# Performance work log

Measured on AMD Instinct MI355X. Metric: run time of the kernel, lower is better.

## Reference

```python
import jax, jax.numpy as jnp
import numpy as np

B, N, H = 8, 2048, 1024

def setup_inputs() -> dict:
    key = jax.random.key(0)
    ks = jax.random.split(key, 10)
    s = 1.0 / np.sqrt(2 * H)
    return {
        "sem": jax.random.normal(ks[0], (B, N, H), jnp.float32),
        "temp": jax.random.normal(ks[1], (B, N, H), jnp.float32),
        "Wq": jax.random.normal(ks[2], (2 * H, H), jnp.float32) * s,
        "bq": jnp.zeros((H,), jnp.float32),
        "Wk": jax.random.normal(ks[3], (2 * H, H), jnp.float32) * s,
        "bk": jnp.zeros((H,), jnp.float32),
        "Wv": jax.random.normal(ks[4], (2 * H, H), jnp.float32) * s,
        "bv": jnp.zeros((H,), jnp.float32),
        "Wg": jax.random.normal(ks[5], (2 * H, 1), jnp.float32) * s,
        "bg": jnp.zeros((1,), jnp.float32),
    }

def reference(sem, temp, Wq, bq, Wk, bk, Wv, bv, Wg, bg):
    combined = jnp.concatenate([sem, temp], axis=-1)          # [B,N,2H]
    Q = combined @ Wq + bq                                    # [B,N,H]
    K = combined @ Wk + bk
    V = combined @ Wv + bv
    scale = 1.0 / jnp.sqrt(jnp.asarray(Q.shape[-1], Q.dtype))
    scores = jnp.einsum('bqh,bkh->bqk', Q, K) * scale         # [B,N,N]
    attn = jax.nn.softmax(scores, axis=-1)
    gate = jax.nn.sigmoid(combined @ Wg + bg)                 # [B,N,1]
    attn_weights = attn * gate                                # row-wise gate
    fused = jnp.einsum('bqk,bkh->bqh', attn_weights, V)       # [B,N,H]
    return fused + sem, attn_weights.mean(axis=1)             # [B,N,H], [B,N]
```

## Files before the change

### kernel.cpp

```cpp
#include <hip/hip_runtime.h>
#include <stdint.h>
#include <math.h>

#define NB 8
#define NN 2048
#define HH 1024
#define K2 2048
#define MM 16384

typedef unsigned short u16;
typedef __attribute__((ext_vector_type(8))) short short8v;
typedef __attribute__((ext_vector_type(4))) float floatx4;

__device__ __forceinline__ float bf2f(u16 u) { return __uint_as_float(((unsigned)u) << 16); }
__device__ __forceinline__ u16 f2bf(float f) {
  unsigned u = __float_as_uint(f);
  unsigned r = (u + 0x7fffu + ((u >> 16) & 1u)) >> 16;
  return (u16)r;
}

__device__ __forceinline__ void async16(const void* g, void* lds) {
  __builtin_amdgcn_global_load_lds((const __attribute__((address_space(1))) void*)g,
                                   (__attribute__((address_space(3))) void*)lds,
                                   16, 0, 0);
}

__device__ __forceinline__ int xcd_swz(int bid, int nblk) {
  return (bid & 7) * (nblk >> 3) + (bid >> 3);
}

#define SBAR() __builtin_amdgcn_sched_barrier(0)

__device__ __forceinline__ void gemm128_core(const u16* __restrict__ A, int lda,
                                             const u16* __restrict__ Bt, int ldb,
                                             int rowA0, int rowB0, int K,
                                             u16* sA, u16* sB, floatx4 acc[4][4]) {
  const int t = threadIdx.x;
  const int w = t >> 6, l = t & 63;
  const int wr = w >> 1, wc = w & 1;

#pragma unroll
  for (int mi = 0; mi < 4; mi++)
#pragma unroll
    for (int ni = 0; ni < 4; ni++) { floatx4 z = {0.f,0.f,0.f,0.f}; acc[mi][ni] = z; }

  const int srow = l >> 2;
  const int cs = (((l & 3) ^ ((l >> 3) & 3)) << 3);
  const u16* gA0 = A + (size_t)(rowA0 + w * 32 + srow) * lda + cs;
  const u16* gA1 = A + (size_t)(rowA0 + w * 32 + 16 + srow) * lda + cs;
  const u16* gB0 = Bt + (size_t)(rowB0 + w * 32 + srow) * ldb + cs;
  const u16* gB1 = Bt + (size_t)(rowB0 + w * 32 + 16 + srow) * ldb + cs;
  char* dA = (char*)sA + w * 2048 + l * 16;
  char* dB = (char*)sB + w * 2048 + l * 16;

  const int fr = l & 15;
  const int ch = (((l >> 4) ^ ((fr >> 1) & 3)) << 4);
  const int abase = wr * 4096 + fr * 64 + ch;
  const int bbase = wc * 4096 + fr * 64 + ch;

  const int NT = K >> 5;

#define STG128(bi, kt) { const int ko_ = (kt) << 5; const int bo_ = (bi) << 13; \
    async16(gA0 + ko_, dA + bo_); async16(gA1 + ko_, dA + bo_ + 1024);          \
    async16(gB0 + ko_, dB + bo_); async16(gB1 + ko_, dB + bo_ + 1024); }

  STG128(0, 0);
  for (int tt = 0; tt < NT; ++tt) {
    const int bc = tt & 1;
    if (tt + 1 < NT) {
      STG128(bc ^ 1, tt + 1);
      asm volatile("s_waitcnt vmcnt(4)" ::: "memory");
    } else {
      asm volatile("s_waitcnt vmcnt(0)" ::: "memory");
    }
    __builtin_amdgcn_s_barrier();

    const char* a = (const char*)sA + (bc << 13);
    const char* b = (const char*)sB + (bc << 13);
    short8v af[4], bf[4];
#pragma unroll
    for (int mi = 0; mi < 4; mi++) af[mi] = *(const short8v*)(a + abase + mi * 1024);
#pragma unroll
    for (int ni = 0; ni < 4; ni++) bf[ni] = *(const short8v*)(b + bbase + ni * 1024);
    __builtin_amdgcn_s_setprio(1);
#pragma unroll
    for (int mi = 0; mi < 4; mi++)
#pragma unroll
      for (int ni = 0; ni < 4; ni++)
        acc[mi][ni] = __builtin_amdgcn_mfma_f32_16x16x32_bf16(af[mi], bf[ni], acc[mi][ni], 0, 0, 0);
    __builtin_amdgcn_s_setprio(0);
    SBAR();
    __builtin_amdgcn_s_barrier();
  }
#undef STG128
}

__global__ void __launch_bounds__(256) k_prep_gate(const float* __restrict__ sem,
                                                   const float* __restrict__ temp,
                                                   const float* __restrict__ Wg,
                                                   const float* __restrict__ bg,
                                                   u16* __restrict__ X, float* __restrict__ gate) {
  __shared__ float red[4];
  int t = threadIdx.x, w = t >> 6, l = t & 63;
  float4 wa = *(const float4*)(Wg + t * 4);
  float4 wb = *(const float4*)(Wg + 1024 + t * 4);
  float bgv = bg[0];
  int row0 = blockIdx.x * 8;
  for (int rr = 0; rr < 8; rr++) {
    int row = row0 + rr;
    const float* s0 = sem + (size_t)row * 1024 + t * 4;
    const float* t0 = temp + (size_t)row * 1024 + t * 4;
    u16* xr = X + (size_t)row * 2048;
    float4 a = *(const float4*)s0;
    float4 b = *(const float4*)t0;
    ushort4 oa = { f2bf(a.x), f2bf(a.y), f2bf(a.z), f2bf(a.w) };
    ushort4 ob = { f2bf(b.x), f2bf(b.y), f2bf(b.z), f2bf(b.w) };
    *(ushort4*)(xr + t * 4) = oa;
    *(ushort4*)(xr + 1024 + t * 4) = ob;
    float s = a.x * wa.x + a.y * wa.y + a.z * wa.z + a.w * wa.w
            + b.x * wb.x + b.y * wb.y + b.z * wb.z + b.w * wb.w;
#pragma unroll
    for (int off = 32; off > 0; off >>= 1) s += __shfl_xor(s, off);
    if (l == 0) red[w] = s;
    __syncthreads();
    if (t == 0) {
      float tot = red[0] + red[1] + red[2] + red[3] + bgv;
      gate[row] = 1.f / (1.f + expf(-tot));
    }
    __syncthreads();
  }
}

__global__ void __launch_bounds__(256) k_transpose_w3(const float* __restrict__ Wq,
                                                      const float* __restrict__ Wk,
                                                      const float* __restrict__ Wv,
                                                      u16* __restrict__ Wt) {
  __shared__ float s[32][33];
  int tile = blockIdx.x;
  int which = tile >> 11; tile &= 2047;
  const float* W = which == 0 ? Wq : which == 1 ? Wk : Wv;
  u16* dst = Wt + (size_t)which * 1024 * 2048;
  int nt = tile & 31, kt = tile >> 5;
  int tx = threadIdx.x & 31, ty = threadIdx.x >> 5;
  int n0 = nt << 5, k0 = kt << 5;
#pragma unroll
  for (int j = 0; j < 32; j += 8)
    s[ty + j][tx] = W[(size_t)(k0 + ty + j) * 1024 + (n0 + tx)];
  __syncthreads();
#pragma unroll
  for (int j = 0; j < 32; j += 8)
    dst[(size_t)(n0 + ty + j) * 2048 + (k0 + tx)] = f2bf(s[tx][ty + j]);
}

__global__ void __launch_bounds__(256, 4) k_proj_qkv(const u16* __restrict__ X,
                                                     const u16* __restrict__ Wt,
                                                     const float* __restrict__ bq,
                                                     const float* __restrict__ bk,
                                                     const float* __restrict__ bv,
                                                     u16* __restrict__ Qb,
                                                     u16* __restrict__ Kb,
                                                     u16* __restrict__ Vt) {
  __shared__ __align__(16) u16 sA[2 * 4096];
  __shared__ __align__(16) u16 sB[2 * 4096];
  int tile = xcd_swz(blockIdx.x, 3072);
  int bm = tile / 24, bn = tile - bm * 24;
  floatx4 acc[4][4];
  gemm128_core(X, K2, Wt, K2, bm * 128, bn * 128, K2, sA, sB, acc);

  const int t = threadIdx.x, w = t >> 6, l = t & 63;
  const int wr = w >> 1, wc = w & 1;
  const int r0 = bm * 128 + wr * 64 + ((l >> 4) << 2);
  const int c0 = (bn & 7) * 128 + wc * 64 + (l & 15);
  const int which = bn >> 3;
  if (which == 2) {
#pragma unroll
    for (int ni = 0; ni < 4; ni++) {
      int h = c0 + ni * 16;
      float bvv = bv[h];
#pragma unroll
      for (int mi = 0; mi < 4; mi++) {
        int rg = r0 + mi * 16;
        int b = rg >> 11, n = rg & 2047;
        ushort4 o = { f2bf(acc[mi][ni][0] + bvv), f2bf(acc[mi][ni][1] + bvv),
                      f2bf(acc[mi][ni][2] + bvv), f2bf(acc[mi][ni][3] + bvv) };
        *(ushort4*)&Vt[((size_t)b * 1024 + h) * 2048 + n] = o;
      }
    }
  } else {
    u16* Out = (which == 0) ? Qb : Kb;
    const float* bias = (which == 0) ? bq : bk;
#pragma unroll
    for (int ni = 0; ni < 4; ni++) {
      int c1 = c0 + ni * 16;
      float bvv = bias[c1];
#pragma unroll
      for (int mi = 0; mi < 4; mi++)
#pragma unroll
        for (int i = 0; i < 4; i++)
          Out[(size_t)(r0 + mi * 16 + i) * 1024 + c1] = f2bf(acc[mi][ni][i] + bvv);
    }
  }
}

__global__ void __launch_bounds__(256, 4) k_scores(const u16* __restrict__ Q, const u16* __restrict__ Kb,
                                                   u16* __restrict__ E, float* __restrict__ lsum) {
  __shared__ __align__(16) u16 sA[2 * 4096];
  __shared__ __align__(16) u16 sB[2 * 4096];
  int tile = xcd_swz(blockIdx.x, 2048);
  int b = tile >> 8, r = tile & 255, bm = r >> 4, bn = r & 15;
  const u16* A = Q + (size_t)b * NN * HH;
  const u16* Bt = Kb + (size_t)b * NN * HH;
  floatx4 acc[4][4];
  gemm128_core(A, HH, Bt, HH, bm * 128, bn * 128, HH, sA, sB, acc);

  u16* Eb = E + (size_t)b * NN * NN;
  float* lb = lsum + b * NN;
  const int t = threadIdx.x, w = t >> 6, l = t & 63;
  const int wr = w >> 1, wc = w & 1;
  const int q0 = bm * 128 + wr * 64 + ((l >> 4) << 2);
  const int k0c = bn * 128 + wc * 64 + (l & 15);
#pragma unroll
  for (int mi = 0; mi < 4; mi++)
#pragma unroll
    for (int i = 0; i < 4; i++) {
      int q = q0 + mi * 16 + i;
      float rs = 0.f;
#pragma unroll
      for (int ni = 0; ni < 4; ni++) {
        float e = expf(acc[mi][ni][i] * 0.03125f);
        Eb[(size_t)q * NN + k0c + ni * 16] = f2bf(e);
        rs += e;
      }
      rs += __shfl_xor(rs, 1);
      rs += __shfl_xor(rs, 2);
      rs += __shfl_xor(rs, 4);
      rs += __shfl_xor(rs, 8);
      if ((l & 15) == 0) atomicAdd(&lb[q], rs);
    }
}

__global__ void __launch_bounds__(256, 4) k_pv(const u16* __restrict__ E, const u16* __restrict__ Vt,
                                               const float* __restrict__ gate, const float* __restrict__ lsum,
                                               const float* __restrict__ sem, float* __restrict__ out) {
  __shared__ __align__(16) u16 sA[2 * 4096];
  __shared__ __align__(16) u16 sB[2 * 4096];
  int tile = xcd_swz(blockIdx.x, 1024);
  int b = tile >> 7, r = tile & 127, bm = r >> 3, bn = r & 7;
  const u16* A = E + (size_t)b * NN * NN;
  const u16* Bt = Vt + (size_t)b * HH * NN;
  floatx4 acc[4][4];
  gemm128_core(A, NN, Bt, NN, bm * 128, bn * 128, NN, sA, sB, acc);

  const int t = threadIdx.x, w = t >> 6, l = t & 63;
  const int wr = w >> 1, wc = w & 1;
  const int q0 = bm * 128 + wr * 64 + ((l >> 4) << 2);
  const int h0 = bn * 128 + wc * 64 + (l & 15);
#pragma unroll
  for (int mi = 0; mi < 4; mi++)
#pragma unroll
    for (int i = 0; i < 4; i++) {
      int q = q0 + mi * 16 + i;
      size_t gq = (size_t)b * NN + q;
      float wq = gate[gq] / lsum[gq];
#pragma unroll
      for (int ni = 0; ni < 4; ni++) {
        int h = h0 + ni * 16;
        out[gq * HH + h] = acc[mi][ni][i] * wq + sem[gq * HH + h];
      }
    }
}

__global__ void __launch_bounds__(256) k_colmean(const u16* __restrict__ E, const float* __restrict__ gate,
                                                 const float* __restrict__ lsum, float* __restrict__ cm) {
  __shared__ float wsh[256];
  int bid = blockIdx.x;
  int b = bid >> 5, rest = bid & 31;
  int ks = rest >> 3, qc = rest & 7;
  int t = threadIdx.x;
  {
    size_t gq = (size_t)b * NN + qc * 256 + t;
    wsh[t] = gate[gq] / lsum[gq];
  }
  __syncthreads();
  const u16* Eb = E + ((size_t)b * NN + (size_t)qc * 256) * NN + ks * 512 + 2 * t;
  float s0 = 0.f, s1 = 0.f;
#pragma unroll 4
  for (int q = 0; q < 256; q++) {
    unsigned v = *(const unsigned*)(Eb + (size_t)q * NN);
    float wq = wsh[q];
    s0 += wq * __uint_as_float(v << 16);
    s1 += wq * __uint_as_float(v & 0xffff0000u);
  }
  float* c = cm + b * NN + ks * 512 + 2 * t;
  atomicAdd(c, s0 * (1.f / 2048.f));
  atomicAdd(c + 1, s1 * (1.f / 2048.f));
}

extern "C" void kernel_launch(void* const* d_in, const int* in_sizes, int n_in,
                              void* d_out, int out_size, void* d_ws, size_t ws_size,
                              hipStream_t stream) {
  const float* sem  = (const float*)d_in[0];
  const float* temp = (const float*)d_in[1];
  const float* Wq   = (const float*)d_in[2];
  const float* bq   = (const float*)d_in[3];
  const float* Wk   = (const float*)d_in[4];
  const float* bk   = (const float*)d_in[5];
  const float* Wv   = (const float*)d_in[6];
  const float* bv   = (const float*)d_in[7];
  const float* Wg   = (const float*)d_in[8];
  const float* bg   = (const float*)d_in[9];
  float* out = (float*)d_out;

  char* ws = (char*)d_ws;
  u16* X      = (u16*)ws;
  u16* E      = X;
  u16* WqkvT  = (u16*)(ws + 67108864);
  u16* Qb     = (u16*)(ws + 79691776);
  u16* Kb     = (u16*)(ws + 113246208);
  u16* Vt     = (u16*)(ws + 146800640);
  float* gate = (float*)(ws + 180355072);
  float* lsum = (float*)(ws + 180420608);

  hipMemsetAsync(lsum, 0, 65536, stream);
  hipMemsetAsync(out + 16777216, 0, 65536, stream);

  k_prep_gate<<<2048, 256, 0, stream>>>(sem, temp, Wg, bg, X, gate);
  k_transpose_w3<<<6144, 256, 0, stream>>>(Wq, Wk, Wv, WqkvT);
  k_proj_qkv<<<3072, 256, 0, stream>>>(X, WqkvT, bq, bk, bv, Qb, Kb, Vt);
  k_scores<<<2048, 256, 0, stream>>>(Qb, Kb, E, lsum);
  k_pv<<<1024, 256, 0, stream>>>(E, Vt, gate, lsum, sem, out);
  k_colmean<<<256, 256, 0, stream>>>(E, gate, lsum, out + 16777216);
}
```

Measured before the change: 502.6 us.

## Store Q, K, V and exp-scores as FP8 and run attention GEMMs with FP8 MFMA

```diff
diff --git a/kernel.cpp b/kernel.cpp
--- a/kernel.cpp
+++ b/kernel.cpp
@@ -9,6 +9,7 @@
 #define MM 16384
 
 typedef unsigned short u16;
+typedef unsigned char u8;
 typedef __attribute__((ext_vector_type(8))) short short8v;
 typedef __attribute__((ext_vector_type(4))) float floatx4;
 
@@ -17,6 +18,33 @@
   unsigned u = __float_as_uint(f);
   unsigned r = (u + 0x7fffu + ((u >> 16) & 1u)) >> 16;
   return (u16)r;
+}
+
+__device__ __forceinline__ u8 f2fp8(float f) {
+  unsigned u = __float_as_uint(f);
+  unsigned sgn = (u >> 24) & 0x80u;
+  unsigned mag = u & 0x7fffffffu;
+  if (mag >= 0x43E80000u) return (u8)(sgn | 0x7Eu);
+  int e = (int)(mag >> 23) - 127;
+  unsigned m = mag & 0x7fffffu;
+  if (e < -6) {
+    float af = __uint_as_float(mag);
+    int q = (int)(af * 512.f + 0.5f);
+    if (q >= 8) return (u8)(sgn | 0x08u);
+    return (u8)(sgn | (unsigned)q);
+  }
+  unsigned r = m + 0x7FFFFu + ((m >> 20) & 1u);
+  unsigned m3 = r >> 20;
+  if (m3 >= 8u) { m3 = 0u; e++; }
+  if (e > 8 || (e == 8 && m3 == 7u)) return (u8)(sgn | 0x7Eu);
+  return (u8)(sgn | ((unsigned)(e + 7) << 3) | m3);
+}
+
+__device__ __forceinline__ float fp8dec(int x) {
+  int e = (x >> 3) & 15, m = x & 7;
+  float v = e ? __uint_as_float(((unsigned)(e - 7 + 127) << 23) | ((unsigned)m << 20))
+              : (float)m * 0.001953125f;
+  return (x & 0x80) ? -v : v;
 }
 
 __device__ __forceinline__ void async16(const void* g, void* lds) {
@@ -93,6 +121,84 @@
     __builtin_amdgcn_s_barrier();
   }
 #undef STG128
+}
+
+__device__ __forceinline__ void gemm128_fp8(const u8* __restrict__ A, int lda,
+                                            const u8* __restrict__ Bt, int ldb,
+                                            int rowA0, int rowB0, int K,
+                                            u8* sA, u8* sB, floatx4 acc[4][4]) {
+  const int t = threadIdx.x;
+  const int w = t >> 6, l = t & 63;
+  const int wr = w >> 1, wc = w & 1;
+
+#pragma unroll
+  for (int mi = 0; mi < 4; mi++)
+#pragma unroll
+    for (int ni = 0; ni < 4; ni++) { floatx4 z = {0.f,0.f,0.f,0.f}; acc[mi][ni] = z; }
+
+  const int srow = l >> 2;
+  const int cs = (((l & 3) ^ ((l >> 3) & 3)) << 4);
+  const u8* gA0 = A + (size_t)(rowA0 + w * 32 + srow) * lda + cs;
+  const u8* gA1 = A + (size_t)(rowA0 + w * 32 + 16 + srow) * lda + cs;
+  const u8* gB0 = Bt + (size_t)(rowB0 + w * 32 + srow) * ldb + cs;
+  const u8* gB1 = Bt + (size_t)(rowB0 + w * 32 + 16 + srow) * ldb + cs;
+  char* dA = (char*)sA + w * 2048 + l * 16;
+  char* dB = (char*)sB + w * 2048 + l * 16;
+
+  const int fr = l & 15;
+  const int g = l >> 4;
+  const int x = (fr >> 1) & 3;
+  const int c0 = ((((g >> 1) ^ x) << 4) | ((g & 1) << 3));
+  const int c1 = ((((2 + (g >> 1)) ^ x) << 4) | ((g & 1) << 3));
+  const int arow = wr * 4096 + fr * 64;
+  const int brow = wc * 4096 + fr * 64;
+
+  const int NT = K >> 6;
+
+#define STGF(bi, kt) { const int ko_ = (kt) << 6; const int bo_ = (bi) << 13; \
+    async16(gA0 + ko_, dA + bo_); async16(gA1 + ko_, dA + bo_ + 1024);        \
+    async16(gB0 + ko_, dB + bo_); async16(gB1 + ko_, dB + bo_ + 1024); }
+
+  STGF(0, 0);
+  for (int tt = 0; tt < NT; ++tt) {
+    const int bc = tt & 1;
+    if (tt + 1 < NT) {
+      STGF(bc ^ 1, tt + 1);
+      asm volatile("s_waitcnt vmcnt(4)" ::: "memory");
+    } else {
+      asm volatile("s_waitcnt vmcnt(0)" ::: "memory");
+    }
+    __builtin_amdgcn_s_barrier();
+
+    const char* a = (const char*)sA + (bc << 13);
+    const char* b = (const char*)sB + (bc << 13);
+    long a0[4], a1[4], b0[4], b1[4];
+#pragma unroll
+    for (int mi = 0; mi < 4; mi++) {
+      a0[mi] = *(const long*)(a + arow + mi * 1024 + c0);
+      a1[mi] = *(const long*)(a + arow + mi * 1024 + c1);
+    }
+#pragma unroll
+    for (int ni = 0; ni < 4; ni++) {
+      b0[ni] = *(const long*)(b + brow + ni * 1024 + c0);
+      b1[ni] = *(const long*)(b + brow + ni * 1024 + c1);
+    }
+    __builtin_amdgcn_s_setprio(1);
+#pragma unroll
+    for (int mi = 0; mi < 4; mi++)
+#pragma unroll
+      for (int ni = 0; ni < 4; ni++)
+        acc[mi][ni] = __builtin_amdgcn_mfma_f32_16x16x32_fp8_fp8(a0[mi], b0[ni], acc[mi][ni], 0, 0, 0);
+#pragma unroll
+    for (int mi = 0; mi < 4; mi++)
+#pragma unroll
+      for (int ni = 0; ni < 4; ni++)
+        acc[mi][ni] = __builtin_amdgcn_mfma_f32_16x16x32_fp8_fp8(a1[mi], b1[ni], acc[mi][ni], 0, 0, 0);
+    __builtin_amdgcn_s_setprio(0);
+    SBAR();
+    __builtin_amdgcn_s_barrier();
+  }
+#undef STGF
 }
 
 __global__ void __launch_bounds__(256) k_prep_gate(const float* __restrict__ sem,
@@ -157,9 +263,9 @@
                                                      const float* __restrict__ bq,
                                                      const float* __restrict__ bk,
                                                      const float* __restrict__ bv,
-                                                     u16* __restrict__ Qb,
-                                                     u16* __restrict__ Kb,
-                                                     u16* __restrict__ Vt) {
+                                                     u8* __restrict__ Qb,
+                                                     u8* __restrict__ Kb,
+                                                     u8* __restrict__ Vt) {
   __shared__ __align__(16) u16 sA[2 * 4096];
   __shared__ __align__(16) u16 sB[2 * 4096];
   int tile = xcd_swz(blockIdx.x, 3072);
@@ -181,13 +287,13 @@
       for (int mi = 0; mi < 4; mi++) {
         int rg = r0 + mi * 16;
         int b = rg >> 11, n = rg & 2047;
-        ushort4 o = { f2bf(acc[mi][ni][0] + bvv), f2bf(acc[mi][ni][1] + bvv),
-                      f2bf(acc[mi][ni][2] + bvv), f2bf(acc[mi][ni][3] + bvv) };
-        *(ushort4*)&Vt[((size_t)b * 1024 + h) * 2048 + n] = o;
+        uchar4 o = { f2fp8(acc[mi][ni][0] + bvv), f2fp8(acc[mi][ni][1] + bvv),
+                     f2fp8(acc[mi][ni][2] + bvv), f2fp8(acc[mi][ni][3] + bvv) };
+        *(uchar4*)&Vt[((size_t)b * 1024 + h) * 2048 + n] = o;
       }
     }
   } else {
-    u16* Out = (which == 0) ? Qb : Kb;
+    u8* Out = (which == 0) ? Qb : Kb;
     const float* bias = (which == 0) ? bq : bk;
 #pragma unroll
     for (int ni = 0; ni < 4; ni++) {
@@ -197,23 +303,23 @@
       for (int mi = 0; mi < 4; mi++)
 #pragma unroll
         for (int i = 0; i < 4; i++)
-          Out[(size_t)(r0 + mi * 16 + i) * 1024 + c1] = f2bf(acc[mi][ni][i] + bvv);
-    }
-  }
-}
-
-__global__ void __launch_bounds__(256, 4) k_scores(const u16* __restrict__ Q, const u16* __restrict__ Kb,
-                                                   u16* __restrict__ E, float* __restrict__ lsum) {
-  __shared__ __align__(16) u16 sA[2 * 4096];
-  __shared__ __align__(16) u16 sB[2 * 4096];
+          Out[(size_t)(r0 + mi * 16 + i) * 1024 + c1] = f2fp8(acc[mi][ni][i] + bvv);
+    }
+  }
+}
+
+__global__ void __launch_bounds__(256, 4) k_scores(const u8* __restrict__ Q, const u8* __restrict__ Kb,
+                                                   u8* __restrict__ E, float* __restrict__ lsum) {
+  __shared__ __align__(16) u8 sA[2 * 8192];
+  __shared__ __align__(16) u8 sB[2 * 8192];
   int tile = xcd_swz(blockIdx.x, 2048);
   int b = tile >> 8, r = tile & 255, bm = r >> 4, bn = r & 15;
-  const u16* A = Q + (size_t)b * NN * HH;
-  const u16* Bt = Kb + (size_t)b * NN * HH;
+  const u8* A = Q + (size_t)b * NN * HH;
+  const u8* Bt = Kb + (size_t)b * NN * HH;
   floatx4 acc[4][4];
-  gemm128_core(A, HH, Bt, HH, bm * 128, bn * 128, HH, sA, sB, acc);
-
-  u16* Eb = E + (size_t)b * NN * NN;
+  gemm128_fp8(A, HH, Bt, HH, bm * 128, bn * 128, HH, sA, sB, acc);
+
+  u8* Eb = E + (size_t)b * NN * NN;
   float* lb = lsum + b * NN;
   const int t = threadIdx.x, w = t >> 6, l = t & 63;
   const int wr = w >> 1, wc = w & 1;
@@ -228,8 +334,9 @@
 #pragma unroll
       for (int ni = 0; ni < 4; ni++) {
         float e = expf(acc[mi][ni][i] * 0.03125f);
-        Eb[(size_t)q * NN + k0c + ni * 16] = f2bf(e);
-        rs += e;
+        u8 c = f2fp8(e * 0.25f);
+        Eb[(size_t)q * NN + k0c + ni * 16] = c;
+        rs += fp8dec(c);
       }
       rs += __shfl_xor(rs, 1);
       rs += __shfl_xor(rs, 2);
@@ -239,17 +346,17 @@
     }
 }
 
-__global__ void __launch_bounds__(256, 4) k_pv(const u16* __restrict__ E, const u16* __restrict__ Vt,
+__global__ void __launch_bounds__(256, 4) k_pv(const u8* __restrict__ E, const u8* __restrict__ Vt,
                                                const float* __restrict__ gate, const float* __restrict__ lsum,
                                                const float* __restrict__ sem, float* __restrict__ out) {
-  __shared__ __align__(16) u16 sA[2 * 4096];
-  __shared__ __align__(16) u16 sB[2 * 4096];
+  __shared__ __align__(16) u8 sA[2 * 8192];
+  __shared__ __align__(16) u8 sB[2 * 8192];
   int tile = xcd_swz(blockIdx.x, 1024);
   int b = tile >> 7, r = tile & 127, bm = r >> 3, bn = r & 7;
-  const u16* A = E + (size_t)b * NN * NN;
-  const u16* Bt = Vt + (size_t)b * HH * NN;
+  const u8* A = E + (size_t)b * NN * NN;
+  const u8* Bt = Vt + (size_t)b * HH * NN;
   floatx4 acc[4][4];
-  gemm128_core(A, NN, Bt, NN, bm * 128, bn * 128, NN, sA, sB, acc);
+  gemm128_fp8(A, NN, Bt, NN, bm * 128, bn * 128, NN, sA, sB, acc);
 
   const int t = threadIdx.x, w = t >> 6, l = t & 63;
   const int wr = w >> 1, wc = w & 1;
@@ -270,30 +377,37 @@
     }
 }
 
-__global__ void __launch_bounds__(256) k_colmean(const u16* __restrict__ E, const float* __restrict__ gate,
+__global__ void __launch_bounds__(256) k_colmean(const u8* __restrict__ E, const float* __restrict__ gate,
                                                  const float* __restrict__ lsum, float* __restrict__ cm) {
   __shared__ float wsh[256];
+  __shared__ float lut[256];
   int bid = blockIdx.x;
-  int b = bid >> 5, rest = bid & 31;
+  int b = bid >> 4, rest = bid & 15;
   int ks = rest >> 3, qc = rest & 7;
   int t = threadIdx.x;
+  lut[t] = fp8dec(t);
   {
     size_t gq = (size_t)b * NN + qc * 256 + t;
-    wsh[t] = gate[gq] / lsum[gq];
+    wsh[t] = gate[gq] / lsum[gq] * (1.f / 2048.f);
   }
   __syncthreads();
-  const u16* Eb = E + ((size_t)b * NN + (size_t)qc * 256) * NN + ks * 512 + 2 * t;
-  float s0 = 0.f, s1 = 0.f;
+  int k0 = ks * 1024 + 4 * t;
+  const u8* Eb = E + ((size_t)b * NN + (size_t)qc * 256) * NN + k0;
+  float s0 = 0.f, s1 = 0.f, s2 = 0.f, s3 = 0.f;
 #pragma unroll 4
   for (int q = 0; q < 256; q++) {
-    unsigned v = *(const unsigned*)(Eb + (size_t)q * NN);
+    uchar4 v = *(const uchar4*)(Eb + (size_t)q * NN);
     float wq = wsh[q];
-    s0 += wq * __uint_as_float(v << 16);
-    s1 += wq * __uint_as_float(v & 0xffff0000u);
-  }
-  float* c = cm + b * NN + ks * 512 + 2 * t;
-  atomicAdd(c, s0 * (1.f / 2048.f));
-  atomicAdd(c + 1, s1 * (1.f / 2048.f));
+    s0 += wq * lut[v.x];
+    s1 += wq * lut[v.y];
+    s2 += wq * lut[v.z];
+    s3 += wq * lut[v.w];
+  }
+  float* c = cm + b * NN + k0;
+  atomicAdd(c + 0, s0);
+  atomicAdd(c + 1, s1);
+  atomicAdd(c + 2, s2);
+  atomicAdd(c + 3, s3);
 }
 
 extern "C" void kernel_launch(void* const* d_in, const int* in_sizes, int n_in,
@@ -313,13 +427,13 @@
 
   char* ws = (char*)d_ws;
   u16* X      = (u16*)ws;
-  u16* E      = X;
+  u8*  E      = (u8*)ws;
   u16* WqkvT  = (u16*)(ws + 67108864);
-  u16* Qb     = (u16*)(ws + 79691776);
-  u16* Kb     = (u16*)(ws + 113246208);
-  u16* Vt     = (u16*)(ws + 146800640);
-  float* gate = (float*)(ws + 180355072);
-  float* lsum = (float*)(ws + 180420608);
+  u8*  Qb     = (u8*)(ws + 79691776);
+  u8*  Kb     = (u8*)(ws + 96468992);
+  u8*  Vt     = (u8*)(ws + 113246208);
+  float* gate = (float*)(ws + 130023424);
+  float* lsum = (float*)(ws + 130088960);
 
   hipMemsetAsync(lsum, 0, 65536, stream);
   hipMemsetAsync(out + 16777216, 0, 65536, stream);
@@ -329,5 +443,5 @@
   k_proj_qkv<<<3072, 256, 0, stream>>>(X, WqkvT, bq, bk, bv, Qb, Kb, Vt);
   k_scores<<<2048, 256, 0, stream>>>(Qb, Kb, E, lsum);
   k_pv<<<1024, 256, 0, stream>>>(E, Vt, gate, lsum, sem, out);
-  k_colmean<<<256, 256, 0, stream>>>(E, gate, lsum, out + 16777216);
-}
+  k_colmean<<<128, 256, 0, stream>>>(E, gate, lsum, out + 16777216);
+}
```

New measurement: 570.3 us. +13.5%, slower.
